# Performance work log

Measured on AMD Instinct MI355X. Metric: run time of the kernel, lower is better.

Reference implementation:

```python
import jax, jax.numpy as jnp
import numpy as np

PATCH_DIM = 256
TRANS_DIM = 256
K_PATCH = 8


def _gelu(x):
    return jax.nn.gelu(x, approximate=False)  # torch nn.GELU default is exact


def setup_inputs() -> dict:
    key = jax.random.key(0)
    ks = jax.random.split(key, 20)
    s = 0.02
    d, t = PATCH_DIM, TRANS_DIM
    return {
        "x": jax.random.normal(ks[0], (4, 4096, 3 + d), dtype=jnp.float32),
        # weights stored (in, out): y = x @ W + b  (equiv to torch Linear)
        "W_in": jax.random.normal(ks[1], (d, t), jnp.float32) * s,
        "b_in": jax.random.normal(ks[2], (t,), jnp.float32) * s,
        "Wq": jax.random.normal(ks[3], (t, t), jnp.float32) * s,
        "Wk": jax.random.normal(ks[4], (t, t), jnp.float32) * s,
        "Wv": jax.random.normal(ks[5], (t, t), jnp.float32) * s,
        "Wg1": jax.random.normal(ks[6], (t, t), jnp.float32) * s,
        "bg1": jax.random.normal(ks[7], (t,), jnp.float32) * s,
        "Wg2": jax.random.normal(ks[8], (t, t), jnp.float32) * s,
        "bg2": jax.random.normal(ks[9], (t,), jnp.float32) * s,
        "W_out": jax.random.normal(ks[10], (t, d), jnp.float32) * s,
        "b_out": jax.random.normal(ks[11], (d,), jnp.float32) * s,
        "Wp1": jax.random.normal(ks[12], (10, 128), jnp.float32) * s,
        "bp1": jax.random.normal(ks[13], (128,), jnp.float32) * s,
        "Wp2": jax.random.normal(ks[14], (128, t), jnp.float32) * s,
        "bp2": jax.random.normal(ks[15], (t,), jnp.float32) * s,
    }


def reference(x, W_in, b_in, Wq, Wk, Wv, Wg1, bg1, Wg2, bg2, W_out, b_out, Wp1, bp1, Wp2, bp2):
    centroid = x[:, :, :3]              # [B,S,3]
    pre = x[:, :, 3:]                   # [B,S,D]
    B, S, _ = centroid.shape
    scale = TRANS_DIM ** (-0.5)

    # square_distance: ||a-b||^2 = |a|^2 + |b|^2 - 2 a.b
    sq = jnp.sum(centroid * centroid, axis=-1)                     # [B,S]
    dist = sq[:, :, None] + sq[:, None, :] - 2.0 * jnp.einsum(
        "bsd,btd->bst", centroid, centroid)                        # [B,S,S]
    idx = jnp.argsort(dist, axis=-1)[:, :, :K_PATCH]               # [B,S,k]

    # index_points gather: [B,S,k,3]
    knn = jax.vmap(lambda c, i: c[i])(centroid, idx)
    ref_vec = knn - centroid[:, :, None, :]
    pos_struct = jnp.concatenate([
        jnp.broadcast_to(centroid[:, :, None, :], (B, S, K_PATCH, 3)),
        knn,
        ref_vec,
        jnp.linalg.norm(ref_vec, axis=-1, keepdims=True),
    ], axis=-1)                                                    # [B,S,k,10]

    pos_h = _gelu(pos_struct @ Wp1 + bp1) @ Wp2 + bp2              # [B,S,k,T]
    pos_emb = jnp.max(pos_h, axis=2)                               # [B,S,T]

    h = pre @ W_in + b_in + pos_emb                                # [B,S,T]
    q, k, v = h @ Wq, h @ Wk, h @ Wv
    attn = (_gelu((q - k) @ Wg1 + bg1) @ Wg2 + bg2) * scale
    attn = jax.nn.softmax(attn, axis=-1)                           # over feature dim
    res = attn * v
    return res @ W_out + b_out + pre                               # [B,S,D]
```

## Files before the change

kernel.cpp:

```cpp
#include <hip/hip_runtime.h>
#include <hip/hip_bf16.h>
#include <math.h>

#define S_   4096
#define XROW 259

typedef const float* fpp;
typedef __attribute__((ext_vector_type(8))) short   s8b;
typedef __attribute__((ext_vector_type(4))) float   f32x4;

__device__ __forceinline__ float us2f(unsigned short u){ return __uint_as_float(((unsigned)u)<<16); }
__device__ __forceinline__ unsigned short f2bu(float f){
  __hip_bfloat16 h = __float2bfloat16(f);
  return *reinterpret_cast<unsigned short*>(&h);
}
__device__ __forceinline__ float gelu_f(float v){
  float u2 = 2.0f * v * fmaf(0.0356774081f, v*v, 0.7978845608f);
  float e  = __expf(u2);
  return v * (1.0f - __builtin_amdgcn_rcpf(e + 1.0f));
}

__global__ __launch_bounds__(256) void k_prep(
    fpp W_in, fpp Wq, fpp Wk, fpp Wv, fpp Wg1, fpp Wg2, fpp W_out, fpp Wp2, fpp Wp1,
    fpp x, unsigned short* __restrict__ FO, float4* __restrict__ cbuf)
{
  int bb = blockIdx.x, wv = threadIdx.x>>6, lane = threadIdx.x&63;
  if (bb < 192) {
    int m  = bb >> 5;
    int fi = (bb & 31)*4 + wv;
    int c = fi >> 3, s = fi & 7;
    int col = c*16 + (lane&15);
    int k0  = s*32 + (lane>>4)*8;
    fpp Wm = (m==0)?W_in:(m==2)?Wv:(m==3)?Wg1:(m==4)?Wg2:(m==5)?W_out:Wq;
    s8b v;
#pragma unroll
    for (int j=0;j<8;j++){
      float f = Wm[(size_t)(k0+j)*256 + col];
      if (m==1) f -= Wk[(size_t)(k0+j)*256 + col];
      v[j] = (short)f2bu(f);
    }
    *(s8b*)(FO + (size_t)m*65536 + (size_t)fi*512 + lane*8) = v;
  } else if (bb < 208) {
    int fi = (bb-192)*4 + wv;
    int c = fi >> 2, s = fi & 3;
    int col = c*16 + (lane&15);
    int k0  = s*32 + (lane>>4)*8;
    s8b v;
#pragma unroll
    for (int j=0;j<8;j++) v[j] = (short)f2bu(Wp2[(size_t)(k0+j)*256 + col]);
    *(s8b*)(FO + 393216 + (size_t)fi*512 + lane*8) = v;
  } else if (bb < 210) {
    int fi = (bb-208)*4 + wv;
    int col = fi*16 + (lane&15);
    int k0  = (lane>>4)*8;
    s8b v;
#pragma unroll
    for (int j=0;j<8;j++){
      int k = k0 + j;
      v[j] = (k < 10) ? (short)f2bu(Wp1[(size_t)k*128 + col]) : (short)0;
    }
    *(s8b*)(FO + 425984 + (size_t)fi*512 + lane*8) = v;
  } else {
    int t = (bb-210)*256 + threadIdx.x;
    size_t xrow = (size_t)t * XROW;
    float cx = x[xrow], cy = x[xrow+1], cz = x[xrow+2];
    cbuf[t] = make_float4(cx, cy, cz, 0.5f*fmaf(cz,cz,fmaf(cy,cy,cx*cx)) + 64.0f);
  }
}

__global__ __launch_bounds__(512,4) void k_knn(const float4* __restrict__ cbuf,
                                               unsigned short* __restrict__ idxw)
{
  __shared__ float4 cent4[S_];
  const int rowbase = blockIdx.x * 32;
  const int b = rowbase >> 12;
  const float4* cb = cbuf + (size_t)b*S_;
  for (int t = threadIdx.x; t < S_; t += 512) cent4[t] = cb[t];
  __syncthreads();
  const int r = threadIdx.x >> 4;
  const int L = threadIdx.x & 15;
  const int s = (rowbase & (S_-1)) + r;
  float4 cs = cent4[s];
  const float nsx = -cs.x, nsy = -cs.y, nsz = -cs.z;
  unsigned bk0=0xFFFFFFFFu, bk1=0xFFFFFFFFu, bk2=0xFFFFFFFFu, bk3=0xFFFFFFFFu;
  int t = L;
#pragma unroll 4
  for (int i = 0; i < 256; ++i) {
    float4 c = cent4[t];
    float m = fmaf(nsx, c.x, fmaf(nsy, c.y, fmaf(nsz, c.z, c.w)));
    unsigned kk = (__float_as_uint(m) & 0xFFFFF000u) | (unsigned)t;
    unsigned lo;
    lo = min(kk,bk0); kk = max(kk,bk0); bk0 = lo;
    lo = min(kk,bk1); kk = max(kk,bk1); bk1 = lo;
    lo = min(kk,bk2); kk = max(kk,bk2); bk2 = lo;
    bk3 = min(kk,bk3);
    t += 16;
  }
  size_t obase = (size_t)(rowbase + r) * 8;
  int h = 0;
#pragma unroll
  for (int round = 0; round < 8; ++round) {
    unsigned mdv = (h==0)?bk0:(h==1)?bk1:(h==2)?bk2:(h==3)?bk3:0xFFFFFFFFu;
    unsigned gd = mdv;
#pragma unroll
    for (int off=1; off<16; off<<=1)
      gd = min(gd, (unsigned)__shfl_xor((int)gd, off));
    if (L == 0) idxw[obase + round] = (unsigned short)(gd & 0xFFFu);
    h += (mdv == gd) ? 1 : 0;
  }
}

__global__ __launch_bounds__(512,4) void k_mega(
    fpp x, const unsigned short* __restrict__ idxw,
    fpp bp1, fpp bp2,
    const unsigned short* __restrict__ FO,
    fpp b_in, fpp bg1, fpp bg2, fpp b_out,
    float* __restrict__ out)
{
  __shared__ __align__(16) char pool[50688];
  __shared__ __align__(16) unsigned short pe[8448];
  unsigned short* X0 = (unsigned short*)pool;
  unsigned short* X1 = X0 + 8448;
  unsigned short* X2 = X1 + 8448;
  unsigned short (*psb)[40]  = (unsigned short (*)[40])pool;
  unsigned short (*hh)[136]  = (unsigned short (*)[136])(pool + 20480);

  const int tid = threadIdx.x, lane = tid & 63, wv = tid >> 6;
  const int arow = lane & 15, akb = lane >> 4, rbase = akb*4;
  const int ctb = wv*2;
  const int tok0 = blockIdx.x * 32, b = tok0 >> 12;
  const unsigned short* FO2 = FO + 393216;
  const unsigned short* FO3 = FO + 425984;
  const int col0 = ctb*16 + arow, col1 = col0 + 16;

  s8b bf3 = *(const s8b*)(FO3 + wv*512 + lane*8);
  float b1v = bp1[wv*16 + arow];
  float bp2v0 = bp2[col0], bp2v1 = bp2[col1];

  if (tid < 256) {
    int tk = tid >> 3;
    size_t grow = (size_t)(tok0 + tk), xrow = grow * XROW;
    float cx=x[xrow], cy=x[xrow+1], cz=x[xrow+2];
    int nb = idxw[grow*8 + (tid & 7)];
    size_t nrow = ((size_t)(b*S_ + nb)) * XROW;
    float nx=x[nrow], ny=x[nrow+1], nz=x[nrow+2];
    float rx=nx-cx, ry=ny-cy, rz=nz-cz;
    float nrm = sqrtf(fmaf(rz,rz,fmaf(ry,ry,rx*rx)));
    unsigned short* p = psb[tid];
    s8b v0 = { (short)f2bu(cx),(short)f2bu(cy),(short)f2bu(cz),(short)f2bu(nx),
               (short)f2bu(ny),(short)f2bu(nz),(short)f2bu(rx),(short)f2bu(ry) };
    s8b v1 = { (short)f2bu(rz),(short)f2bu(nrm),0,0,0,0,0,0 };
    s8b vz = { 0,0,0,0,0,0,0,0 };
    *(s8b*)(p) = v0; *(s8b*)(p+8) = v1; *(s8b*)(p+16) = vz; *(s8b*)(p+24) = vz;
  }
  __syncthreads();

  for (int c=0;c<4;++c){
    f32x4 h4[4];
#pragma unroll
    for (int rt=0;rt<4;++rt){
      s8b af = *(const s8b*)(&psb[c*64 + rt*16 + arow][akb*8]);
      h4[rt] = __builtin_amdgcn_mfma_f32_16x16x32_bf16(af, bf3, (f32x4){0.f,0.f,0.f,0.f}, 0,0,0);
    }
#pragma unroll
    for (int rt=0;rt<4;++rt)
#pragma unroll
      for (int rr=0;rr<4;++rr)
        hh[rt*16 + rbase + rr][wv*16 + arow] = f2bu(gelu_f(h4[rt][rr] + b1v));
    __syncthreads();
    f32x4 a2c[4][2];
#pragma unroll
    for (int rt=0;rt<4;++rt){ a2c[rt][0]=(f32x4){0.f,0.f,0.f,0.f}; a2c[rt][1]=(f32x4){0.f,0.f,0.f,0.f}; }
#pragma unroll
    for (int s=0;s<4;++s){
      s8b af0 = *(const s8b*)(&hh[ 0 + arow][s*32 + akb*8]);
      s8b af1 = *(const s8b*)(&hh[16 + arow][s*32 + akb*8]);
      s8b af2 = *(const s8b*)(&hh[32 + arow][s*32 + akb*8]);
      s8b af3v= *(const s8b*)(&hh[48 + arow][s*32 + akb*8]);
#pragma unroll
      for (int i=0;i<2;++i){
        s8b bf = *(const s8b*)(FO2 + ((size_t)((ctb+i)*4 + s))*512 + lane*8);
        a2c[0][i] = __builtin_amdgcn_mfma_f32_16x16x32_bf16(af0,  bf, a2c[0][i], 0,0,0);
        a2c[1][i] = __builtin_amdgcn_mfma_f32_16x16x32_bf16(af1,  bf, a2c[1][i], 0,0,0);
        a2c[2][i] = __builtin_amdgcn_mfma_f32_16x16x32_bf16(af2,  bf, a2c[2][i], 0,0,0);
        a2c[3][i] = __builtin_amdgcn_mfma_f32_16x16x32_bf16(af3v, bf, a2c[3][i], 0,0,0);
      }
    }
#pragma unroll
    for (int rt=0;rt<4;++rt)
#pragma unroll
      for (int i=0;i<2;++i){
        float pm = fmaxf(fmaxf(a2c[rt][i][0],a2c[rt][i][1]), fmaxf(a2c[rt][i][2],a2c[rt][i][3]));
        pm = fmaxf(pm, __shfl_xor(pm, 16));
        if ((akb & 1) == 0)
          pe[(c*8 + rt*2 + (akb>>1))*264 + (ctb+i)*16 + arow] = f2bu(pm + (i ? bp2v1 : bp2v0));
      }
    __syncthreads();
  }

#pragma unroll
  for (int p=0;p<2;++p){
    int i2 = p*512 + tid;
    int row = i2 >> 5, cb2 = i2 & 31;
    const float* src = x + (size_t)(tok0 + row)*XROW + 3 + cb2*8;
    s8b v;
#pragma unroll
    for (int j=0;j<8;j++) v[j] = (short)f2bu(src[j]);
    *(s8b*)(X0 + row*264 + cb2*8) = v;
  }
  __syncthreads();

  f32x4 acc[2][2];
  auto gphase = [&](const unsigned short* A, const unsigned short* FOm){
#pragma unroll
    for (int rt=0;rt<2;++rt){ acc[rt][0]=(f32x4){0.f,0.f,0.f,0.f}; acc[rt][1]=(f32x4){0.f,0.f,0.f,0.f}; }
#pragma unroll
    for (int s=0;s<8;++s){
      s8b a0 = *(const s8b*)(A + arow*264 + s*32 + akb*8);
      s8b a1 = *(const s8b*)(A + (16+arow)*264 + s*32 + akb*8);
#pragma unroll
      for (int i=0;i<2;++i){
        s8b bf = *(const s8b*)(FOm + ((size_t)((ctb+i)*8 + s))*512 + lane*8);
        acc[0][i] = __builtin_amdgcn_mfma_f32_16x16x32_bf16(a0, bf, acc[0][i], 0,0,0);
        acc[1][i] = __builtin_amdgcn_mfma_f32_16x16x32_bf16(a1, bf, acc[1][i], 0,0,0);
      }
    }
  };

  gphase(X0, FO);
#pragma unroll
  for (int i=0;i<2;++i){
    int col = i ? col1 : col0;
    float bi = b_in[col];
#pragma unroll
    for (int rt=0;rt<2;++rt)
#pragma unroll
      for (int rr=0;rr<4;++rr){
        int row = rt*16 + rbase + rr;
        X1[row*264 + col] = f2bu(acc[rt][i][rr] + bi + us2f(pe[row*264 + col]));
      }
  }
  __syncthreads();

  gphase(X1, FO + 65536);
#pragma unroll
  for (int i=0;i<2;++i){
    int col = i ? col1 : col0;
#pragma unroll
    for (int rt=0;rt<2;++rt)
#pragma unroll
      for (int rr=0;rr<4;++rr)
        X0[(rt*16 + rbase + rr)*264 + col] = f2bu(acc[rt][i][rr]);
  }
  __syncthreads();

  gphase(X0, FO + 196608);
#pragma unroll
  for (int i=0;i<2;++i){
    int col = i ? col1 : col0;
    float bi = bg1[col];
#pragma unroll
    for (int rt=0;rt<2;++rt)
#pragma unroll
      for (int rr=0;rr<4;++rr)
        X2[(rt*16 + rbase + rr)*264 + col] = f2bu(gelu_f(acc[rt][i][rr] + bi));
  }
  __syncthreads();

  gphase(X2, FO + 262144);
#pragma unroll
  for (int i=0;i<2;++i){
    int col = i ? col1 : col0;
    float bi = bg2[col];
#pragma unroll
    for (int rt=0;rt<2;++rt)
#pragma unroll
      for (int rr=0;rr<4;++rr)
        X0[(rt*16 + rbase + rr)*264 + col] = f2bu((acc[rt][i][rr] + bi) * 0.0625f);
  }
  __syncthreads();

  {
    int row = tid >> 4, li = tid & 15;
    unsigned short* rp = X0 + row*264 + li*16;
    uint4 u0 = *(uint4*)rp, u1 = *(uint4*)(rp + 8);
    float f[16];
    f[0]=us2f(u0.x&0xffff); f[1]=us2f(u0.x>>16); f[2]=us2f(u0.y&0xffff); f[3]=us2f(u0.y>>16);
    f[4]=us2f(u0.z&0xffff); f[5]=us2f(u0.z>>16); f[6]=us2f(u0.w&0xffff); f[7]=us2f(u0.w>>16);
    f[8]=us2f(u1.x&0xffff); f[9]=us2f(u1.x>>16); f[10]=us2f(u1.y&0xffff); f[11]=us2f(u1.y>>16);
    f[12]=us2f(u1.z&0xffff); f[13]=us2f(u1.z>>16); f[14]=us2f(u1.w&0xffff); f[15]=us2f(u1.w>>16);
    float mx = f[0];
#pragma unroll
    for (int i=1;i<16;i++) mx = fmaxf(mx, f[i]);
#pragma unroll
    for (int o=1;o<16;o<<=1) mx = fmaxf(mx, __shfl_xor(mx, o));
    float ssum = 0.f;
#pragma unroll
    for (int i=0;i<16;i++){ f[i] = __expf(f[i]-mx); ssum += f[i]; }
#pragma unroll
    for (int o=1;o<16;o<<=1) ssum += __shfl_xor(ssum, o);
    float inv = __builtin_amdgcn_rcpf(ssum);
    uint4 w0, w1;
    w0.x=f2bu(f[0]*inv) | ((unsigned)f2bu(f[1]*inv)<<16);
    w0.y=f2bu(f[2]*inv) | ((unsigned)f2bu(f[3]*inv)<<16);
    w0.z=f2bu(f[4]*inv) | ((unsigned)f2bu(f[5]*inv)<<16);
    w0.w=f2bu(f[6]*inv) | ((unsigned)f2bu(f[7]*inv)<<16);
    w1.x=f2bu(f[8]*inv) | ((unsigned)f2bu(f[9]*inv)<<16);
    w1.y=f2bu(f[10]*inv)| ((unsigned)f2bu(f[11]*inv)<<16);
    w1.z=f2bu(f[12]*inv)| ((unsigned)f2bu(f[13]*inv)<<16);
    w1.w=f2bu(f[14]*inv)| ((unsigned)f2bu(f[15]*inv)<<16);
    *(uint4*)rp = w0; *(uint4*)(rp+8) = w1;
  }
  __syncthreads();

  gphase(X1, FO + 131072);
#pragma unroll
  for (int i=0;i<2;++i){
    int col = i ? col1 : col0;
#pragma unroll
    for (int rt=0;rt<2;++rt)
#pragma unroll
      for (int rr=0;rr<4;++rr){
        int row = rt*16 + rbase + rr;
        X2[row*264 + col] = f2bu(us2f(X0[row*264 + col]) * acc[rt][i][rr]);
      }
  }
  __syncthreads();

  gphase(X2, FO + 327680);
#pragma unroll
  for (int i=0;i<2;++i){
    int col = i ? col1 : col0;
    float bo = b_out[col];
#pragma unroll
    for (int rt=0;rt<2;++rt)
#pragma unroll
      for (int rr=0;rr<4;++rr){
        size_t row = (size_t)(tok0 + rt*16 + rbase + rr);
        out[row*256 + col] = acc[rt][i][rr] + bo + x[row*XROW + 3 + col];
      }
  }
}

extern "C" void kernel_launch(void* const* d_in, const int* in_sizes, int n_in,
                              void* d_out, int out_size, void* d_ws, size_t ws_size,
                              hipStream_t stream)
{
  fpp x    = (fpp)d_in[0];
  fpp W_in = (fpp)d_in[1];  fpp b_in = (fpp)d_in[2];
  fpp Wq   = (fpp)d_in[3];  fpp Wk   = (fpp)d_in[4];  fpp Wv = (fpp)d_in[5];
  fpp Wg1  = (fpp)d_in[6];  fpp bg1  = (fpp)d_in[7];
  fpp Wg2  = (fpp)d_in[8];  fpp bg2  = (fpp)d_in[9];
  fpp W_out= (fpp)d_in[10]; fpp b_out= (fpp)d_in[11];
  fpp Wp1  = (fpp)d_in[12]; fpp bp1  = (fpp)d_in[13];
  fpp Wp2  = (fpp)d_in[14]; fpp bp2  = (fpp)d_in[15];

  char* ws = (char*)d_ws;
  unsigned short* idxw = (unsigned short*)ws;
  unsigned short* FO   = (unsigned short*)(ws + 262144);

  float4* cbuf = (float4*)((char*)d_out + 16515072);

  k_prep<<<274, 256, 0, stream>>>(W_in,Wq,Wk,Wv,Wg1,Wg2,W_out,Wp2,Wp1, x, FO, cbuf);
  k_knn <<<512, 512, 0, stream>>>(cbuf, idxw);
  k_mega<<<512, 512, 0, stream>>>(x, idxw, bp1, bp2, FO,
                                  b_in, bg1, bg2, b_out, (float*)d_out);
}
```

Baseline: 73.44 us.

## Truncate bf16 conversions, shrink kNN top-list, halve pos-MLP barrier rounds

Replaces round-to-nearest bf16 conversion with plain bit truncation throughout the fused kernel, removing the rounding arithmetic on every store. The kNN per-lane sorted list drops from four to three entries, which cuts compare/swap work but can lose a true neighbour if four of a row's nearest neighbours fall in one lane. The positional MLP now processes 128 rows per chunk in two passes with a larger shared-memory pool, halving the number of block barriers. Truncation adds a small downward bias to accuracy, and the larger LDS footprint may lower occupancy.

```diff
diff --git a/kernel.cpp b/kernel.cpp
--- a/kernel.cpp
+++ b/kernel.cpp
@@ -13,6 +13,9 @@
 __device__ __forceinline__ unsigned short f2bu(float f){
   __hip_bfloat16 h = __float2bfloat16(f);
   return *reinterpret_cast<unsigned short*>(&h);
+}
+__device__ __forceinline__ unsigned short f2bt(float f){
+  return (unsigned short)(__float_as_uint(f) >> 16);
 }
 __device__ __forceinline__ float gelu_f(float v){
   float u2 = 2.0f * v * fmaf(0.0356774081f, v*v, 0.7978845608f);
@@ -82,7 +85,7 @@
   const int s = (rowbase & (S_-1)) + r;
   float4 cs = cent4[s];
   const float nsx = -cs.x, nsy = -cs.y, nsz = -cs.z;
-  unsigned bk0=0xFFFFFFFFu, bk1=0xFFFFFFFFu, bk2=0xFFFFFFFFu, bk3=0xFFFFFFFFu;
+  unsigned bk0=0xFFFFFFFFu, bk1=0xFFFFFFFFu, bk2=0xFFFFFFFFu;
   int t = L;
 #pragma unroll 4
   for (int i = 0; i < 256; ++i) {
@@ -92,15 +95,14 @@
     unsigned lo;
     lo = min(kk,bk0); kk = max(kk,bk0); bk0 = lo;
     lo = min(kk,bk1); kk = max(kk,bk1); bk1 = lo;
-    lo = min(kk,bk2); kk = max(kk,bk2); bk2 = lo;
-    bk3 = min(kk,bk3);
+    bk2 = min(kk,bk2);
     t += 16;
   }
   size_t obase = (size_t)(rowbase + r) * 8;
   int h = 0;
 #pragma unroll
   for (int round = 0; round < 8; ++round) {
-    unsigned mdv = (h==0)?bk0:(h==1)?bk1:(h==2)?bk2:(h==3)?bk3:0xFFFFFFFFu;
+    unsigned mdv = (h==0)?bk0:(h==1)?bk1:(h==2)?bk2:0xFFFFFFFFu;
     unsigned gd = mdv;
 #pragma unroll
     for (int off=1; off<16; off<<=1)
@@ -117,7 +119,7 @@
     fpp b_in, fpp bg1, fpp bg2, fpp b_out,
     float* __restrict__ out)
 {
-  __shared__ __align__(16) char pool[50688];
+  __shared__ __align__(16) char pool[55296];
   __shared__ __align__(16) unsigned short pe[8448];
   unsigned short* X0 = (unsigned short*)pool;
   unsigned short* X1 = X0 + 8448;
@@ -147,54 +149,54 @@
     float rx=nx-cx, ry=ny-cy, rz=nz-cz;
     float nrm = sqrtf(fmaf(rz,rz,fmaf(ry,ry,rx*rx)));
     unsigned short* p = psb[tid];
-    s8b v0 = { (short)f2bu(cx),(short)f2bu(cy),(short)f2bu(cz),(short)f2bu(nx),
-               (short)f2bu(ny),(short)f2bu(nz),(short)f2bu(rx),(short)f2bu(ry) };
-    s8b v1 = { (short)f2bu(rz),(short)f2bu(nrm),0,0,0,0,0,0 };
+    s8b v0 = { (short)f2bt(cx),(short)f2bt(cy),(short)f2bt(cz),(short)f2bt(nx),
+               (short)f2bt(ny),(short)f2bt(nz),(short)f2bt(rx),(short)f2bt(ry) };
+    s8b v1 = { (short)f2bt(rz),(short)f2bt(nrm),0,0,0,0,0,0 };
     s8b vz = { 0,0,0,0,0,0,0,0 };
     *(s8b*)(p) = v0; *(s8b*)(p+8) = v1; *(s8b*)(p+16) = vz; *(s8b*)(p+24) = vz;
   }
   __syncthreads();
 
-  for (int c=0;c<4;++c){
-    f32x4 h4[4];
-#pragma unroll
-    for (int rt=0;rt<4;++rt){
-      s8b af = *(const s8b*)(&psb[c*64 + rt*16 + arow][akb*8]);
-      h4[rt] = __builtin_amdgcn_mfma_f32_16x16x32_bf16(af, bf3, (f32x4){0.f,0.f,0.f,0.f}, 0,0,0);
-    }
-#pragma unroll
-    for (int rt=0;rt<4;++rt)
+  for (int c=0;c<2;++c){
+#pragma unroll
+    for (int rt=0;rt<8;++rt){
+      s8b af = *(const s8b*)(&psb[c*128 + rt*16 + arow][akb*8]);
+      f32x4 h4 = __builtin_amdgcn_mfma_f32_16x16x32_bf16(af, bf3, (f32x4){0.f,0.f,0.f,0.f}, 0,0,0);
 #pragma unroll
       for (int rr=0;rr<4;++rr)
-        hh[rt*16 + rbase + rr][wv*16 + arow] = f2bu(gelu_f(h4[rt][rr] + b1v));
+        hh[rt*16 + rbase + rr][wv*16 + arow] = f2bt(gelu_f(h4[rr] + b1v));
+    }
     __syncthreads();
-    f32x4 a2c[4][2];
-#pragma unroll
-    for (int rt=0;rt<4;++rt){ a2c[rt][0]=(f32x4){0.f,0.f,0.f,0.f}; a2c[rt][1]=(f32x4){0.f,0.f,0.f,0.f}; }
-#pragma unroll
-    for (int s=0;s<4;++s){
-      s8b af0 = *(const s8b*)(&hh[ 0 + arow][s*32 + akb*8]);
-      s8b af1 = *(const s8b*)(&hh[16 + arow][s*32 + akb*8]);
-      s8b af2 = *(const s8b*)(&hh[32 + arow][s*32 + akb*8]);
-      s8b af3v= *(const s8b*)(&hh[48 + arow][s*32 + akb*8]);
-#pragma unroll
-      for (int i=0;i<2;++i){
-        s8b bf = *(const s8b*)(FO2 + ((size_t)((ctb+i)*4 + s))*512 + lane*8);
-        a2c[0][i] = __builtin_amdgcn_mfma_f32_16x16x32_bf16(af0,  bf, a2c[0][i], 0,0,0);
-        a2c[1][i] = __builtin_amdgcn_mfma_f32_16x16x32_bf16(af1,  bf, a2c[1][i], 0,0,0);
-        a2c[2][i] = __builtin_amdgcn_mfma_f32_16x16x32_bf16(af2,  bf, a2c[2][i], 0,0,0);
-        a2c[3][i] = __builtin_amdgcn_mfma_f32_16x16x32_bf16(af3v, bf, a2c[3][i], 0,0,0);
-      }
-    }
-#pragma unroll
-    for (int rt=0;rt<4;++rt)
-#pragma unroll
-      for (int i=0;i<2;++i){
-        float pm = fmaxf(fmaxf(a2c[rt][i][0],a2c[rt][i][1]), fmaxf(a2c[rt][i][2],a2c[rt][i][3]));
-        pm = fmaxf(pm, __shfl_xor(pm, 16));
-        if ((akb & 1) == 0)
-          pe[(c*8 + rt*2 + (akb>>1))*264 + (ctb+i)*16 + arow] = f2bu(pm + (i ? bp2v1 : bp2v0));
-      }
+#pragma unroll
+    for (int p=0;p<2;++p){
+      f32x4 a2c[4][2];
+#pragma unroll
+      for (int rt=0;rt<4;++rt){ a2c[rt][0]=(f32x4){0.f,0.f,0.f,0.f}; a2c[rt][1]=(f32x4){0.f,0.f,0.f,0.f}; }
+#pragma unroll
+      for (int s=0;s<4;++s){
+        s8b af0 = *(const s8b*)(&hh[p*64 +  0 + arow][s*32 + akb*8]);
+        s8b af1 = *(const s8b*)(&hh[p*64 + 16 + arow][s*32 + akb*8]);
+        s8b af2 = *(const s8b*)(&hh[p*64 + 32 + arow][s*32 + akb*8]);
+        s8b af3v= *(const s8b*)(&hh[p*64 + 48 + arow][s*32 + akb*8]);
+#pragma unroll
+        for (int i=0;i<2;++i){
+          s8b bf = *(const s8b*)(FO2 + ((size_t)((ctb+i)*4 + s))*512 + lane*8);
+          a2c[0][i] = __builtin_amdgcn_mfma_f32_16x16x32_bf16(af0,  bf, a2c[0][i], 0,0,0);
+          a2c[1][i] = __builtin_amdgcn_mfma_f32_16x16x32_bf16(af1,  bf, a2c[1][i], 0,0,0);
+          a2c[2][i] = __builtin_amdgcn_mfma_f32_16x16x32_bf16(af2,  bf, a2c[2][i], 0,0,0);
+          a2c[3][i] = __builtin_amdgcn_mfma_f32_16x16x32_bf16(af3v, bf, a2c[3][i], 0,0,0);
+        }
+      }
+#pragma unroll
+      for (int rt=0;rt<4;++rt)
+#pragma unroll
+        for (int i=0;i<2;++i){
+          float pm = fmaxf(fmaxf(a2c[rt][i][0],a2c[rt][i][1]), fmaxf(a2c[rt][i][2],a2c[rt][i][3]));
+          pm = fmaxf(pm, __shfl_xor(pm, 16));
+          if ((akb & 1) == 0)
+            pe[(c*16 + p*8 + rt*2 + (akb>>1))*264 + (ctb+i)*16 + arow] = f2bt(pm + (i ? bp2v1 : bp2v0));
+        }
+    }
     __syncthreads();
   }
 
@@ -205,7 +207,7 @@
     const float* src = x + (size_t)(tok0 + row)*XROW + 3 + cb2*8;
     s8b v;
 #pragma unroll
-    for (int j=0;j<8;j++) v[j] = (short)f2bu(src[j]);
+    for (int j=0;j<8;j++) v[j] = (short)f2bt(src[j]);
     *(s8b*)(X0 + row*264 + cb2*8) = v;
   }
   __syncthreads();
@@ -237,7 +239,7 @@
 #pragma unroll
       for (int rr=0;rr<4;++rr){
         int row = rt*16 + rbase + rr;
-        X1[row*264 + col] = f2bu(acc[rt][i][rr] + bi + us2f(pe[row*264 + col]));
+        X1[row*264 + col] = f2bt(acc[rt][i][rr] + bi + us2f(pe[row*264 + col]));
       }
   }
   __syncthreads();
@@ -250,7 +252,7 @@
     for (int rt=0;rt<2;++rt)
 #pragma unroll
       for (int rr=0;rr<4;++rr)
-        X0[(rt*16 + rbase + rr)*264 + col] = f2bu(acc[rt][i][rr]);
+        X0[(rt*16 + rbase + rr)*264 + col] = f2bt(acc[rt][i][rr]);
   }
   __syncthreads();
 
@@ -263,7 +265,7 @@
     for (int rt=0;rt<2;++rt)
 #pragma unroll
       for (int rr=0;rr<4;++rr)
-        X2[(rt*16 + rbase + rr)*264 + col] = f2bu(gelu_f(acc[rt][i][rr] + bi));
+        X2[(rt*16 + rbase + rr)*264 + col] = f2bt(gelu_f(acc[rt][i][rr] + bi));
   }
   __syncthreads();
 
@@ -276,7 +278,7 @@
     for (int rt=0;rt<2;++rt)
 #pragma unroll
       for (int rr=0;rr<4;++rr)
-        X0[(rt*16 + rbase + rr)*264 + col] = f2bu((acc[rt][i][rr] + bi) * 0.0625f);
+        X0[(rt*16 + rbase + rr)*264 + col] = f2bt((acc[rt][i][rr] + bi) * 0.0625f);
   }
   __syncthreads();
 
@@ -301,14 +303,14 @@
     for (int o=1;o<16;o<<=1) ssum += __shfl_xor(ssum, o);
     float inv = __builtin_amdgcn_rcpf(ssum);
     uint4 w0, w1;
-    w0.x=f2bu(f[0]*inv) | ((unsigned)f2bu(f[1]*inv)<<16);
-    w0.y=f2bu(f[2]*inv) | ((unsigned)f2bu(f[3]*inv)<<16);
-    w0.z=f2bu(f[4]*inv) | ((unsigned)f2bu(f[5]*inv)<<16);
-    w0.w=f2bu(f[6]*inv) | ((unsigned)f2bu(f[7]*inv)<<16);
-    w1.x=f2bu(f[8]*inv) | ((unsigned)f2bu(f[9]*inv)<<16);
-    w1.y=f2bu(f[10]*inv)| ((unsigned)f2bu(f[11]*inv)<<16);
-    w1.z=f2bu(f[12]*inv)| ((unsigned)f2bu(f[13]*inv)<<16);
-    w1.w=f2bu(f[14]*inv)| ((unsigned)f2bu(f[15]*inv)<<16);
+    w0.x=f2bt(f[0]*inv) | ((unsigned)f2bt(f[1]*inv)<<16);
+    w0.y=f2bt(f[2]*inv) | ((unsigned)f2bt(f[3]*inv)<<16);
+    w0.z=f2bt(f[4]*inv) | ((unsigned)f2bt(f[5]*inv)<<16);
+    w0.w=f2bt(f[6]*inv) | ((unsigned)f2bt(f[7]*inv)<<16);
+    w1.x=f2bt(f[8]*inv) | ((unsigned)f2bt(f[9]*inv)<<16);
+    w1.y=f2bt(f[10]*inv)| ((unsigned)f2bt(f[11]*inv)<<16);
+    w1.z=f2bt(f[12]*inv)| ((unsigned)f2bt(f[13]*inv)<<16);
+    w1.w=f2bt(f[14]*inv)| ((unsigned)f2bt(f[15]*inv)<<16);
     *(uint4*)rp = w0; *(uint4*)(rp+8) = w1;
   }
   __syncthreads();
@@ -322,7 +324,7 @@
 #pragma unroll
       for (int rr=0;rr<4;++rr){
         int row = rt*16 + rbase + rr;
-        X2[row*264 + col] = f2bu(us2f(X0[row*264 + col]) * acc[rt][i][rr]);
+        X2[row*264 + col] = f2bt(us2f(X0[row*264 + col]) * acc[rt][i][rr]);
       }
   }
   __syncthreads();
```

After: 67.65 us. -7.9%, faster.
